# Kernel optimization log

Measured on AMD Instinct MI355X. Metric: run time of the kernel, lower is better.

## Reference

```python
import jax, jax.numpy as jnp
import numpy as np

MARGIN = 2.0
EPS = 1e-9


def setup_inputs() -> dict:
    key = jax.random.key(0)
    k1, k2 = jax.random.split(key)
    N, D, C = 8192, 128, 50
    outputs = jax.random.normal(k1, (N, D), dtype=jnp.float32)
    labels = jax.random.randint(k2, (N,), 0, C, dtype=jnp.int64)
    return {"outputs": outputs, "labels": labels}


def reference(outputs, labels):
    # Pairwise squared distances via Gram trick: ||xi||^2 + ||xj||^2 - 2 xi.xj
    sq = jnp.sum(outputs * outputs, axis=-1)  # [N]
    gram = outputs @ outputs.T                # [N, N]
    dist_sq = jnp.maximum(sq[:, None] + sq[None, :] - 2.0 * gram, 0.0)

    pos = (labels[:, None] == labels[None, :])  # includes i==j, as in original
    num_pos = jnp.sum(pos)
    num_neg = pos.size - num_pos

    dist_pos = jnp.sum(jnp.where(pos, dist_sq, 0.0))
    hinge = jax.nn.relu(MARGIN - jnp.sqrt(dist_sq + EPS))
    dist_neg = jnp.sum(jnp.where(pos, 0.0, hinge * hinge))

    pos_term = jnp.where(num_pos > 0, 0.5 * dist_pos / num_pos, 0.0)
    neg_term = jnp.where(num_neg > 0, 0.5 * dist_neg / num_neg, 0.0)
    return pos_term + neg_term
```

## Files before the change

kernel.cpp:

```cpp
#include <hip/hip_runtime.h>
#include <math.h>

#define NPTS   8192
#define DDIM   128
#define NBLK   64
#define NTRI   2080

using short8 = __attribute__((ext_vector_type(8))) short;
using f32x4  = __attribute__((ext_vector_type(4))) float;

__device__ __forceinline__ unsigned short f2bf(float f) {
    unsigned int u = __float_as_uint(f);
    u += 0x7fffu + ((u >> 16) & 1u);
    return (unsigned short)(u >> 16);
}
__device__ __forceinline__ float bf2f(unsigned short s) {
    return __uint_as_float(((unsigned int)s) << 16);
}

__global__ __launch_bounds__(256) void prep_kernel(
    const float* __restrict__ X, unsigned short* __restrict__ Xbf,
    float* __restrict__ sq)
{
    const int wave = threadIdx.x >> 6, lane = threadIdx.x & 63;
    const int row  = blockIdx.x * 4 + wave;
    float2 v = *(const float2*)(X + (size_t)row * DDIM + lane * 2);
    unsigned short a = f2bf(v.x), b = f2bf(v.y);
    float fa = bf2f(a), fb = bf2f(b);
    float s = fa * fa + fb * fb;
    *(ushort2*)(Xbf + (size_t)row * DDIM + lane * 2) = make_ushort2(a, b);
#pragma unroll
    for (int off = 32; off > 0; off >>= 1) s += __shfl_down(s, off);
    if (lane == 0) sq[row] = s;
}

__global__ __launch_bounds__(256) void pair_kernel(
    const unsigned short* __restrict__ Xbf, const int* __restrict__ lab,
    const float* __restrict__ sq, float* __restrict__ slots )
{
    const int k = blockIdx.x;
    int bi = (int)((129.0f - sqrtf((float)(16641 - 8 * k))) * 0.5f);
    if (bi < 0) bi = 0;
    while (64 * (bi + 1) - ((bi + 1) * bi) / 2 <= k) ++bi;
    while (64 * bi - (bi * (bi - 1)) / 2 > k) --bi;
    const int bj = bi + (k - (64 * bi - (bi * (bi - 1)) / 2));

    __shared__ float sSqA[128], sSqB[128];
    __shared__ int   sLabA[128], sLabB[128];
    __shared__ float rP[4], rN[4];

    const int tid   = threadIdx.x;
    const int rowA0 = bi * 128;
    const int rowB0 = bj * 128;

    if (tid < 128) {
        sSqA[tid]  = sq[rowA0 + tid];
        sLabA[tid] = lab[rowA0 + tid];
    } else {
        int t = tid - 128;
        sSqB[t]  = sq[rowB0 + t];
        sLabB[t] = lab[rowB0 + t];
    }
    __syncthreads();

    const int wave = tid >> 6, lane = tid & 63;
    const int quad = lane >> 4, rr = lane & 15;
    const int wr = wave >> 1, wc = wave & 1;

    const unsigned short* pA = Xbf + (size_t)(rowA0 + wr * 64 + rr) * DDIM + quad * 8;
    const unsigned short* pB = Xbf + (size_t)(rowB0 + wc * 64 + rr) * DDIM + quad * 8;

    f32x4 acc[4][4];
#pragma unroll
    for (int i = 0; i < 4; ++i)
#pragma unroll
        for (int j = 0; j < 4; ++j)
            acc[i][j] = (f32x4){0.f, 0.f, 0.f, 0.f};

#pragma unroll
    for (int kc = 0; kc < 4; ++kc) {
        short8 a[4], b[4];
#pragma unroll
        for (int t = 0; t < 4; ++t)
            a[t] = *(const short8*)(pA + t * 16 * DDIM + kc * 32);
#pragma unroll
        for (int t = 0; t < 4; ++t)
            b[t] = *(const short8*)(pB + t * 16 * DDIM + kc * 32);
#pragma unroll
        for (int i = 0; i < 4; ++i)
#pragma unroll
            for (int j = 0; j < 4; ++j)
                acc[i][j] = __builtin_amdgcn_mfma_f32_16x16x32_bf16(a[i], b[j], acc[i][j], 0, 0, 0);
    }

    float sb[4]; int lbv[4];
#pragma unroll
    for (int j = 0; j < 4; ++j) {
        int cl = wc * 64 + j * 16 + rr;
        sb[j] = sSqB[cl];
        lbv[j] = sLabB[cl];
    }

    float posS = 0.f, dmin = 1e30f;
#pragma unroll
    for (int i = 0; i < 4; ++i) {
#pragma unroll
        for (int rg = 0; rg < 4; ++rg) {
            int   rl = wr * 64 + i * 16 + quad * 4 + rg;
            float sa = sSqA[rl];
            int   la = sLabA[rl];
#pragma unroll
            for (int j = 0; j < 4; ++j) {
                float d = fmaxf(sa + sb[j] - 2.0f * acc[i][j][rg], 0.0f);
                bool same = (la == lbv[j]);
                posS += same ? d : 0.f;
                dmin = fminf(dmin, same ? 1e30f : d);
            }
        }
    }

    float negS = 0.f;
    if (__any(dmin + 1e-9f < 4.0f)) {
#pragma unroll
        for (int i = 0; i < 4; ++i) {
#pragma unroll
            for (int rg = 0; rg < 4; ++rg) {
                int   rl = wr * 64 + i * 16 + quad * 4 + rg;
                float sa = sSqA[rl];
                int   la = sLabA[rl];
#pragma unroll
                for (int j = 0; j < 4; ++j) {
                    float d = fmaxf(sa + sb[j] - 2.0f * acc[i][j][rg], 0.0f);
                    float t = fmaxf(2.0f - sqrtf(d + 1e-9f), 0.f);
                    negS += (la == lbv[j]) ? 0.f : t * t;
                }
            }
        }
    }

    const float factor = (bi == bj) ? 1.0f : 2.0f;
    posS *= factor; negS *= factor;

#pragma unroll
    for (int off = 32; off > 0; off >>= 1) {
        posS += __shfl_down(posS, off);
        negS += __shfl_down(negS, off);
    }
    if (lane == 0) { rP[wave] = posS; rN[wave] = negS; }
    __syncthreads();
    if (tid == 0) {
        slots[k]        = rP[0] + rP[1] + rP[2] + rP[3];
        slots[NTRI + k] = rN[0] + rN[1] + rN[2] + rN[3];
    }
}

__global__ __launch_bounds__(1024) void finalize_kernel(
    const float* __restrict__ slots, const int* __restrict__ lab,
    float* __restrict__ out)
{
    __shared__ int   hist[64];
    __shared__ float sP[16], sN[16];
    const int tid = threadIdx.x;
    if (tid < 64) hist[tid] = 0;
    __syncthreads();
    for (int i = tid; i < NPTS; i += 1024) atomicAdd(&hist[lab[i]], 1);

    float p = 0.f, n = 0.f;
    for (int i = tid; i < NTRI; i += 1024) { p += slots[i]; n += slots[NTRI + i]; }
#pragma unroll
    for (int off = 32; off > 0; off >>= 1) {
        p += __shfl_down(p, off);
        n += __shfl_down(n, off);
    }
    const int wave = tid >> 6, lane = tid & 63;
    if (lane == 0) { sP[wave] = p; sN[wave] = n; }
    __syncthreads();
    if (tid == 0) {
        long long np = 0;
        for (int c = 0; c < 64; ++c) np += (long long)hist[c] * hist[c];
        float tp = 0.f, tn = 0.f;
#pragma unroll
        for (int w = 0; w < 16; ++w) { tp += sP[w]; tn += sN[w]; }
        double dnp = (double)np;
        double dnn = (double)NPTS * (double)NPTS - dnp;
        double pt = (dnp > 0.0) ? 0.5 * (double)tp / dnp : 0.0;
        double nt = (dnn > 0.0) ? 0.5 * (double)tn / dnn : 0.0;
        out[0] = (float)(pt + nt);
    }
}

extern "C" void kernel_launch(void* const* d_in, const int* in_sizes, int n_in,
                              void* d_out, int out_size, void* d_ws, size_t ws_size,
                              hipStream_t stream) {
    const float* X   = (const float*)d_in[0];
    const int*   lab = (const int*)d_in[1];
    float*       out = (float*)d_out;

    char* ws = (char*)d_ws;
    unsigned short* Xbf   = (unsigned short*)(ws);
    float*          sq    = (float*)(ws + 2 * 1024 * 1024);
    float*          slots = (float*)(ws + 2 * 1024 * 1024 + 32 * 1024);

    prep_kernel<<<NPTS / 4, 256, 0, stream>>>(X, Xbf, sq);
    pair_kernel<<<NTRI, 256, 0, stream>>>(Xbf, lab, sq, slots);
    finalize_kernel<<<1, 1024, 0, stream>>>(slots, lab, out);
}
```

Before: 101.9 us.

## Compute positive-pair term from per-class sums and fuse finalize via last-block reduction

Replaces the per-pair positive-distance accumulation with a closed form built from per-class sums, squared norms and counts, which prep_kernel gathers with atomics. The pair kernel then computes only the minimum distance for its early-exit test and the negative hinge sum. A last-block-done counter folds the separate finalize kernel into the pair kernel. All A/B fragments are loaded up front before the MFMA loop, and launch bounds request two blocks per CU. In exchange it adds a memset, many global float atomics in prep, and a closed form in fp32 that can lose precision and differs slightly from using the bf16 Gram values.

```diff
diff --git a/kernel.cpp b/kernel.cpp
--- a/kernel.cpp
+++ b/kernel.cpp
@@ -19,24 +19,43 @@
 }
 
 __global__ __launch_bounds__(256) void prep_kernel(
-    const float* __restrict__ X, unsigned short* __restrict__ Xbf,
-    float* __restrict__ sq)
+    const float* __restrict__ X, const int* __restrict__ lab,
+    unsigned short* __restrict__ Xbf, float* __restrict__ sq,
+    float* __restrict__ clsSum, float* __restrict__ clsSq,
+    int* __restrict__ clsCnt)
 {
     const int wave = threadIdx.x >> 6, lane = threadIdx.x & 63;
     const int row  = blockIdx.x * 4 + wave;
+    const int c    = lab[row];
+
     float2 v = *(const float2*)(X + (size_t)row * DDIM + lane * 2);
     unsigned short a = f2bf(v.x), b = f2bf(v.y);
     float fa = bf2f(a), fb = bf2f(b);
-    float s = fa * fa + fb * fb;
+    float s_bf = fa * fa + fb * fb;
+    float s_fp = v.x * v.x + v.y * v.y;
     *(ushort2*)(Xbf + (size_t)row * DDIM + lane * 2) = make_ushort2(a, b);
-#pragma unroll
-    for (int off = 32; off > 0; off >>= 1) s += __shfl_down(s, off);
-    if (lane == 0) sq[row] = s;
-}
-
-__global__ __launch_bounds__(256) void pair_kernel(
+
+    atomicAdd(&clsSum[c * DDIM + lane * 2],     v.x);
+    atomicAdd(&clsSum[c * DDIM + lane * 2 + 1], v.y);
+
+#pragma unroll
+    for (int off = 32; off > 0; off >>= 1) {
+        s_bf += __shfl_down(s_bf, off);
+        s_fp += __shfl_down(s_fp, off);
+    }
+    if (lane == 0) {
+        sq[row] = s_bf;
+        atomicAdd(&clsSq[c], s_fp);
+        atomicAdd(clsCnt + c, 1);
+    }
+}
+
+__global__ __launch_bounds__(256, 2) void pair_kernel(
     const unsigned short* __restrict__ Xbf, const int* __restrict__ lab,
-    const float* __restrict__ sq, float* __restrict__ slots )
+    const float* __restrict__ sq, float* __restrict__ slots,
+    const float* __restrict__ clsSum, const float* __restrict__ clsSq,
+    const int* __restrict__ clsCnt, unsigned int* __restrict__ counter,
+    float* __restrict__ out)
 {
     const int k = blockIdx.x;
     int bi = (int)((129.0f - sqrtf((float)(16641 - 8 * k))) * 0.5f);
@@ -47,7 +66,8 @@
 
     __shared__ float sSqA[128], sSqB[128];
     __shared__ int   sLabA[128], sLabB[128];
-    __shared__ float rP[4], rN[4];
+    __shared__ float rN[4];
+    __shared__ int   sIsLast;
 
     const int tid   = threadIdx.x;
     const int rowA0 = bi * 128;
@@ -61,7 +81,6 @@
         sSqB[t]  = sq[rowB0 + t];
         sLabB[t] = lab[rowB0 + t];
     }
-    __syncthreads();
 
     const int wave = tid >> 6, lane = tid & 63;
     const int quad = lane >> 4, rr = lane & 15;
@@ -70,6 +89,16 @@
     const unsigned short* pA = Xbf + (size_t)(rowA0 + wr * 64 + rr) * DDIM + quad * 8;
     const unsigned short* pB = Xbf + (size_t)(rowB0 + wc * 64 + rr) * DDIM + quad * 8;
 
+    short8 a[4][4], b[4][4];
+#pragma unroll
+    for (int kc = 0; kc < 4; ++kc) {
+#pragma unroll
+        for (int t = 0; t < 4; ++t) {
+            a[t][kc] = *(const short8*)(pA + t * 16 * DDIM + kc * 32);
+            b[t][kc] = *(const short8*)(pB + t * 16 * DDIM + kc * 32);
+        }
+    }
+
     f32x4 acc[4][4];
 #pragma unroll
     for (int i = 0; i < 4; ++i)
@@ -78,49 +107,37 @@
             acc[i][j] = (f32x4){0.f, 0.f, 0.f, 0.f};
 
 #pragma unroll
-    for (int kc = 0; kc < 4; ++kc) {
-        short8 a[4], b[4];
-#pragma unroll
-        for (int t = 0; t < 4; ++t)
-            a[t] = *(const short8*)(pA + t * 16 * DDIM + kc * 32);
-#pragma unroll
-        for (int t = 0; t < 4; ++t)
-            b[t] = *(const short8*)(pB + t * 16 * DDIM + kc * 32);
+    for (int kc = 0; kc < 4; ++kc)
 #pragma unroll
         for (int i = 0; i < 4; ++i)
 #pragma unroll
             for (int j = 0; j < 4; ++j)
-                acc[i][j] = __builtin_amdgcn_mfma_f32_16x16x32_bf16(a[i], b[j], acc[i][j], 0, 0, 0);
-    }
-
-    float sb[4]; int lbv[4];
-#pragma unroll
-    for (int j = 0; j < 4; ++j) {
-        int cl = wc * 64 + j * 16 + rr;
-        sb[j] = sSqB[cl];
-        lbv[j] = sLabB[cl];
-    }
-
-    float posS = 0.f, dmin = 1e30f;
+                acc[i][j] = __builtin_amdgcn_mfma_f32_16x16x32_bf16(a[i][kc], b[j][kc], acc[i][j], 0, 0, 0);
+
+    __syncthreads();
+
+    float sb[4];
+#pragma unroll
+    for (int j = 0; j < 4; ++j) sb[j] = sSqB[wc * 64 + j * 16 + rr];
+
+    float dmin = 1e30f;
 #pragma unroll
     for (int i = 0; i < 4; ++i) {
-#pragma unroll
-        for (int rg = 0; rg < 4; ++rg) {
-            int   rl = wr * 64 + i * 16 + quad * 4 + rg;
-            float sa = sSqA[rl];
-            int   la = sLabA[rl];
-#pragma unroll
-            for (int j = 0; j < 4; ++j) {
-                float d = fmaxf(sa + sb[j] - 2.0f * acc[i][j][rg], 0.0f);
-                bool same = (la == lbv[j]);
-                posS += same ? d : 0.f;
-                dmin = fminf(dmin, same ? 1e30f : d);
-            }
-        }
+        float sa4[4];
+#pragma unroll
+        for (int rg = 0; rg < 4; ++rg) sa4[rg] = sSqA[wr * 64 + i * 16 + quad * 4 + rg];
+#pragma unroll
+        for (int rg = 0; rg < 4; ++rg)
+#pragma unroll
+            for (int j = 0; j < 4; ++j)
+                dmin = fminf(dmin, sa4[rg] + sb[j] - 2.0f * acc[i][j][rg]);
     }
 
     float negS = 0.f;
-    if (__any(dmin + 1e-9f < 4.0f)) {
+    if (__any(dmin < 4.0f)) {
+        int lb[4];
+#pragma unroll
+        for (int j = 0; j < 4; ++j) lb[j] = sLabB[wc * 64 + j * 16 + rr];
 #pragma unroll
         for (int i = 0; i < 4; ++i) {
 #pragma unroll
@@ -132,60 +149,59 @@
                 for (int j = 0; j < 4; ++j) {
                     float d = fmaxf(sa + sb[j] - 2.0f * acc[i][j][rg], 0.0f);
                     float t = fmaxf(2.0f - sqrtf(d + 1e-9f), 0.f);
-                    negS += (la == lbv[j]) ? 0.f : t * t;
+                    negS += (la == lb[j]) ? 0.f : t * t;
                 }
             }
         }
     }
 
-    const float factor = (bi == bj) ? 1.0f : 2.0f;
-    posS *= factor; negS *= factor;
-
+    negS *= (bi == bj) ? 1.0f : 2.0f;
+#pragma unroll
+    for (int off = 32; off > 0; off >>= 1) negS += __shfl_down(negS, off);
+    if (lane == 0) rN[wave] = negS;
+    __syncthreads();
+    if (tid == 0) {
+        slots[k] = rN[0] + rN[1] + rN[2] + rN[3];
+        __threadfence();
+        unsigned int old = atomicAdd(counter, 1);
+        sIsLast = (old == NTRI - 1);
+    }
+    __syncthreads();
+    if (!sIsLast) return;
+
+    __threadfence();
+    float nsum = 0.f;
+    for (int i = tid; i < NTRI; i += 256) nsum += slots[i];
+#pragma unroll
+    for (int off = 32; off > 0; off >>= 1) nsum += __shfl_down(nsum, off);
+    __syncthreads();
+    if (lane == 0) rN[wave] = nsum;
+    __syncthreads();
+
+    float pp = 0.f, np = 0.f;
+    if (tid < 64) {
+        float s2 = 0.f;
+        for (int d = 0; d < DDIM; ++d) {
+            float v = clsSum[tid * DDIM + d];
+            s2 = fmaf(v, v, s2);
+        }
+        float nc = (float)clsCnt[tid];
+        pp = nc * clsSq[tid] - s2;
+        np = nc * nc;
+    }
 #pragma unroll
     for (int off = 32; off > 0; off >>= 1) {
-        posS += __shfl_down(posS, off);
-        negS += __shfl_down(negS, off);
-    }
-    if (lane == 0) { rP[wave] = posS; rN[wave] = negS; }
-    __syncthreads();
+        pp += __shfl_down(pp, off);
+        np += __shfl_down(np, off);
+    }
     if (tid == 0) {
-        slots[k]        = rP[0] + rP[1] + rP[2] + rP[3];
-        slots[NTRI + k] = rN[0] + rN[1] + rN[2] + rN[3];
-    }
-}
-
-__global__ __launch_bounds__(1024) void finalize_kernel(
-    const float* __restrict__ slots, const int* __restrict__ lab,
-    float* __restrict__ out)
-{
-    __shared__ int   hist[64];
-    __shared__ float sP[16], sN[16];
-    const int tid = threadIdx.x;
-    if (tid < 64) hist[tid] = 0;
-    __syncthreads();
-    for (int i = tid; i < NPTS; i += 1024) atomicAdd(&hist[lab[i]], 1);
-
-    float p = 0.f, n = 0.f;
-    for (int i = tid; i < NTRI; i += 1024) { p += slots[i]; n += slots[NTRI + i]; }
-#pragma unroll
-    for (int off = 32; off > 0; off >>= 1) {
-        p += __shfl_down(p, off);
-        n += __shfl_down(n, off);
-    }
-    const int wave = tid >> 6, lane = tid & 63;
-    if (lane == 0) { sP[wave] = p; sN[wave] = n; }
-    __syncthreads();
-    if (tid == 0) {
-        long long np = 0;
-        for (int c = 0; c < 64; ++c) np += (long long)hist[c] * hist[c];
-        float tp = 0.f, tn = 0.f;
-#pragma unroll
-        for (int w = 0; w < 16; ++w) { tp += sP[w]; tn += sN[w]; }
-        double dnp = (double)np;
-        double dnn = (double)NPTS * (double)NPTS - dnp;
-        double pt = (dnp > 0.0) ? 0.5 * (double)tp / dnp : 0.0;
-        double nt = (dnn > 0.0) ? 0.5 * (double)tn / dnn : 0.0;
-        out[0] = (float)(pt + nt);
+        float  negTotal = rN[0] + rN[1] + rN[2] + rN[3];
+        double dist_pos = 2.0 * (double)pp;
+        double num_pos  = (double)np;
+        double num_neg  = (double)NPTS * (double)NPTS - num_pos;
+        double pos_t = (num_pos > 0.0) ? 0.5 * dist_pos / num_pos : 0.0;
+        double neg_t = (num_neg > 0.0) ? 0.5 * (double)negTotal / num_neg : 0.0;
+        out[0] = (float)(pos_t + neg_t);
     }
 }
 
@@ -197,11 +213,15 @@
     float*       out = (float*)d_out;
 
     char* ws = (char*)d_ws;
-    unsigned short* Xbf   = (unsigned short*)(ws);
-    float*          sq    = (float*)(ws + 2 * 1024 * 1024);
-    float*          slots = (float*)(ws + 2 * 1024 * 1024 + 32 * 1024);
-
-    prep_kernel<<<NPTS / 4, 256, 0, stream>>>(X, Xbf, sq);
-    pair_kernel<<<NTRI, 256, 0, stream>>>(Xbf, lab, sq, slots);
-    finalize_kernel<<<1, 1024, 0, stream>>>(slots, lab, out);
-}
+    unsigned int*   counter = (unsigned int*)(ws + 0);
+    int*            clsCnt  = (int*)(ws + 256);
+    float*          clsSq   = (float*)(ws + 1024);
+    float*          clsSum  = (float*)(ws + 4096);
+    float*          slots   = (float*)(ws + 64 * 1024);
+    float*          sq      = (float*)(ws + 80 * 1024);
+    unsigned short* Xbf     = (unsigned short*)(ws + 128 * 1024);
+
+    hipMemsetAsync(ws, 0, 64 * 1024, stream);
+    prep_kernel<<<NPTS / 4, 256, 0, stream>>>(X, lab, Xbf, sq, clsSum, clsSq, clsCnt);
+    pair_kernel<<<NTRI, 256, 0, stream>>>(Xbf, lab, sq, slots, clsSum, clsSq, clsCnt, counter, out);
+}
```

New measurement: 182.3 us. +78.9%, slower.

## Split pair tiles into per-wave 32x64 triangular tiles and drop LDS staging

Applied to the files above, without the earlier changes.

Each wave now handles its own 32x64 tile of the upper-triangular pair space, with 4 waves per block and 16512 wave tiles in total. Diagonal double counting is removed with an upper-strict mask, and the finalize step drops the 0.5 factor to match. This replaces the per-block shared-memory staging, __syncthreads and cross-wave reduction with direct global loads. The aim is to skip nearly half the redundant diagonal work, gain finer load balance and raise occupancy (launch_bounds 256,4). The cost is reloading B rows per wave instead of sharing them, and more slots for finalize to reduce.

```diff
diff --git a/kernel.cpp b/kernel.cpp
--- a/kernel.cpp
+++ b/kernel.cpp
@@ -3,8 +3,7 @@
 
 #define NPTS   8192
 #define DDIM   128
-#define NBLK   64
-#define NTRI   2080
+#define NT2    16512
 
 using short8 = __attribute__((ext_vector_type(8))) short;
 using f32x4  = __attribute__((ext_vector_type(4))) float;
@@ -16,6 +15,10 @@
 }
 __device__ __forceinline__ float bf2f(unsigned short s) {
     return __uint_as_float(((unsigned int)s) << 16);
+}
+
+__device__ __forceinline__ int Cof(int r) {
+    return 128 * r - ((r * r - 2 * r + (r & 1)) >> 2);
 }
 
 __global__ __launch_bounds__(256) void prep_kernel(
@@ -34,123 +37,113 @@
     if (lane == 0) sq[row] = s;
 }
 
-__global__ __launch_bounds__(256) void pair_kernel(
+__global__ __launch_bounds__(256, 4) void pair_kernel(
     const unsigned short* __restrict__ Xbf, const int* __restrict__ lab,
     const float* __restrict__ sq, float* __restrict__ slots )
 {
-    const int k = blockIdx.x;
-    int bi = (int)((129.0f - sqrtf((float)(16641 - 8 * k))) * 0.5f);
-    if (bi < 0) bi = 0;
-    while (64 * (bi + 1) - ((bi + 1) * bi) / 2 <= k) ++bi;
-    while (64 * bi - (bi * (bi - 1)) / 2 > k) --bi;
-    const int bj = bi + (k - (64 * bi - (bi * (bi - 1)) / 2));
-
-    __shared__ float sSqA[128], sSqB[128];
-    __shared__ int   sLabA[128], sLabB[128];
-    __shared__ float rP[4], rN[4];
-
-    const int tid   = threadIdx.x;
-    const int rowA0 = bi * 128;
-    const int rowB0 = bj * 128;
-
-    if (tid < 128) {
-        sSqA[tid]  = sq[rowA0 + tid];
-        sLabA[tid] = lab[rowA0 + tid];
-    } else {
-        int t = tid - 128;
-        sSqB[t]  = sq[rowB0 + t];
-        sLabB[t] = lab[rowB0 + t];
-    }
-    __syncthreads();
-
-    const int wave = tid >> 6, lane = tid & 63;
+    const int wave = threadIdx.x >> 6, lane = threadIdx.x & 63;
+    const int t = blockIdx.x * 4 + wave;
+
+    float s0 = sqrtf(264196.0f - 16.0f * (float)t);
+    int rb = (int)((514.0f - s0) * 0.5f);
+    if (rb < 0) rb = 0;
+    if (rb > 255) rb = 255;
+    while (Cof(rb + 1) <= t) ++rb;
+    while (Cof(rb) > t) --rb;
+    const int cb = (rb >> 1) + (t - Cof(rb));
+    const bool overlap = (cb == (rb >> 1));
+
     const int quad = lane >> 4, rr = lane & 15;
-    const int wr = wave >> 1, wc = wave & 1;
-
-    const unsigned short* pA = Xbf + (size_t)(rowA0 + wr * 64 + rr) * DDIM + quad * 8;
-    const unsigned short* pB = Xbf + (size_t)(rowB0 + wc * 64 + rr) * DDIM + quad * 8;
-
-    f32x4 acc[4][4];
-#pragma unroll
-    for (int i = 0; i < 4; ++i)
+    const int row0 = rb * 32, col0 = cb * 64;
+
+    const unsigned short* pA = Xbf + (size_t)(row0 + rr) * DDIM + quad * 8;
+    const unsigned short* pB = Xbf + (size_t)(col0 + rr) * DDIM + quad * 8;
+
+    f32x4 acc[2][4];
+#pragma unroll
+    for (int i = 0; i < 2; ++i)
 #pragma unroll
         for (int j = 0; j < 4; ++j)
             acc[i][j] = (f32x4){0.f, 0.f, 0.f, 0.f};
 
 #pragma unroll
     for (int kc = 0; kc < 4; ++kc) {
-        short8 a[4], b[4];
-#pragma unroll
-        for (int t = 0; t < 4; ++t)
-            a[t] = *(const short8*)(pA + t * 16 * DDIM + kc * 32);
-#pragma unroll
-        for (int t = 0; t < 4; ++t)
-            b[t] = *(const short8*)(pB + t * 16 * DDIM + kc * 32);
-#pragma unroll
-        for (int i = 0; i < 4; ++i)
+        short8 a[2], b[4];
+#pragma unroll
+        for (int i = 0; i < 2; ++i)
+            a[i] = *(const short8*)(pA + i * 16 * DDIM + kc * 32);
+#pragma unroll
+        for (int j = 0; j < 4; ++j)
+            b[j] = *(const short8*)(pB + j * 16 * DDIM + kc * 32);
+#pragma unroll
+        for (int i = 0; i < 2; ++i)
 #pragma unroll
             for (int j = 0; j < 4; ++j)
                 acc[i][j] = __builtin_amdgcn_mfma_f32_16x16x32_bf16(a[i], b[j], acc[i][j], 0, 0, 0);
     }
 
-    float sb[4]; int lbv[4];
+    float sb[4]; int lb[4];
 #pragma unroll
     for (int j = 0; j < 4; ++j) {
-        int cl = wc * 64 + j * 16 + rr;
-        sb[j] = sSqB[cl];
-        lbv[j] = sLabB[cl];
-    }
+        int cl = col0 + j * 16 + rr;
+        sb[j] = sq[cl];
+        lb[j] = lab[cl];
+    }
+    float sa[2][4]; int la[2][4];
+#pragma unroll
+    for (int i = 0; i < 2; ++i)
+#pragma unroll
+        for (int rg = 0; rg < 4; ++rg) {
+            int rl = row0 + i * 16 + quad * 4 + rg;
+            sa[i][rg] = sq[rl];
+            la[i][rg] = lab[rl];
+        }
 
     float posS = 0.f, dmin = 1e30f;
 #pragma unroll
-    for (int i = 0; i < 4; ++i) {
+    for (int i = 0; i < 2; ++i) {
 #pragma unroll
         for (int rg = 0; rg < 4; ++rg) {
-            int   rl = wr * 64 + i * 16 + quad * 4 + rg;
-            float sa = sSqA[rl];
-            int   la = sLabA[rl];
+            int rl = row0 + i * 16 + quad * 4 + rg;
 #pragma unroll
             for (int j = 0; j < 4; ++j) {
-                float d = fmaxf(sa + sb[j] - 2.0f * acc[i][j][rg], 0.0f);
-                bool same = (la == lbv[j]);
-                posS += same ? d : 0.f;
-                dmin = fminf(dmin, same ? 1e30f : d);
+                int   cl = col0 + j * 16 + rr;
+                bool  ok = !overlap || (cl > rl);
+                float d0 = sa[i][rg] + sb[j] - 2.0f * acc[i][j][rg];
+                bool  same = (la[i][rg] == lb[j]);
+                posS += (ok && same) ? fmaxf(d0, 0.f) : 0.f;
+                dmin = fminf(dmin, (ok && !same) ? d0 : 1e30f);
             }
         }
     }
 
     float negS = 0.f;
-    if (__any(dmin + 1e-9f < 4.0f)) {
-#pragma unroll
-        for (int i = 0; i < 4; ++i) {
+    if (__any(dmin < 4.0f)) {
+#pragma unroll
+        for (int i = 0; i < 2; ++i) {
 #pragma unroll
             for (int rg = 0; rg < 4; ++rg) {
-                int   rl = wr * 64 + i * 16 + quad * 4 + rg;
-                float sa = sSqA[rl];
-                int   la = sLabA[rl];
+                int rl = row0 + i * 16 + quad * 4 + rg;
 #pragma unroll
                 for (int j = 0; j < 4; ++j) {
-                    float d = fmaxf(sa + sb[j] - 2.0f * acc[i][j][rg], 0.0f);
-                    float t = fmaxf(2.0f - sqrtf(d + 1e-9f), 0.f);
-                    negS += (la == lbv[j]) ? 0.f : t * t;
+                    int   cl = col0 + j * 16 + rr;
+                    bool  ok = !overlap || (cl > rl);
+                    float d = fmaxf(sa[i][rg] + sb[j] - 2.0f * acc[i][j][rg], 0.f);
+                    float h = fmaxf(2.0f - sqrtf(d + 1e-9f), 0.f);
+                    negS += (ok && (la[i][rg] != lb[j])) ? h * h : 0.f;
                 }
             }
         }
     }
 
-    const float factor = (bi == bj) ? 1.0f : 2.0f;
-    posS *= factor; negS *= factor;
-
 #pragma unroll
     for (int off = 32; off > 0; off >>= 1) {
         posS += __shfl_down(posS, off);
         negS += __shfl_down(negS, off);
     }
-    if (lane == 0) { rP[wave] = posS; rN[wave] = negS; }
-    __syncthreads();
-    if (tid == 0) {
-        slots[k]        = rP[0] + rP[1] + rP[2] + rP[3];
-        slots[NTRI + k] = rN[0] + rN[1] + rN[2] + rN[3];
+    if (lane == 0) {
+        slots[t]       = posS;
+        slots[NT2 + t] = negS;
     }
 }
 
@@ -166,7 +159,7 @@
     for (int i = tid; i < NPTS; i += 1024) atomicAdd(&hist[lab[i]], 1);
 
     float p = 0.f, n = 0.f;
-    for (int i = tid; i < NTRI; i += 1024) { p += slots[i]; n += slots[NTRI + i]; }
+    for (int i = tid; i < NT2; i += 1024) { p += slots[i]; n += slots[NT2 + i]; }
 #pragma unroll
     for (int off = 32; off > 0; off >>= 1) {
         p += __shfl_down(p, off);
@@ -181,11 +174,11 @@
         float tp = 0.f, tn = 0.f;
 #pragma unroll
         for (int w = 0; w < 16; ++w) { tp += sP[w]; tn += sN[w]; }
-        double dnp = (double)np;
-        double dnn = (double)NPTS * (double)NPTS - dnp;
-        double pt = (dnp > 0.0) ? 0.5 * (double)tp / dnp : 0.0;
-        double nt = (dnn > 0.0) ? 0.5 * (double)tn / dnn : 0.0;
-        out[0] = (float)(pt + nt);
+        double num_pos = (double)np;
+        double num_neg = (double)NPTS * (double)NPTS - num_pos;
+        double pos_t = (num_pos > 0.0) ? (double)tp / num_pos : 0.0;
+        double neg_t = (num_neg > 0.0) ? (double)tn / num_neg : 0.0;
+        out[0] = (float)(pos_t + neg_t);
     }
 }
 
@@ -197,11 +190,11 @@
     float*       out = (float*)d_out;
 
     char* ws = (char*)d_ws;
-    unsigned short* Xbf   = (unsigned short*)(ws);
-    float*          sq    = (float*)(ws + 2 * 1024 * 1024);
-    float*          slots = (float*)(ws + 2 * 1024 * 1024 + 32 * 1024);
+    float*          slots = (float*)(ws);
+    float*          sq    = (float*)(ws + 160 * 1024);
+    unsigned short* Xbf   = (unsigned short*)(ws + 256 * 1024);
 
     prep_kernel<<<NPTS / 4, 256, 0, stream>>>(X, Xbf, sq);
-    pair_kernel<<<NTRI, 256, 0, stream>>>(Xbf, lab, sq, slots);
+    pair_kernel<<<NT2 / 4, 256, 0, stream>>>(Xbf, lab, sq, slots);
     finalize_kernel<<<1, 1024, 0, stream>>>(slots, lab, out);
 }
```

After: 117.4 us. 1.15x slower.

## Stage tiles via global_load_lds into swizzled LDS and fuse finalize via last-block counter

Applied to the files above, without the earlier changes.

Tiles of the bf16 matrix are copied directly from global into XOR-swizzled shared memory with async LDS loads, and the MFMA operands are then read from LDS instead of being loaded per wave from global memory. The separate finalize kernel is removed: each block atomically increments a counter and the last block does the histogram and final reduction, with the counter cleared by a memset. This is meant to cut duplicate global traffic and one kernel launch. In exchange it uses 64KB of LDS per block, which limits occupancy, and adds a serialized tail reduction in one block.

```diff
diff --git a/kernel.cpp b/kernel.cpp
--- a/kernel.cpp
+++ b/kernel.cpp
@@ -9,6 +9,9 @@
 using short8 = __attribute__((ext_vector_type(8))) short;
 using f32x4  = __attribute__((ext_vector_type(4))) float;
 
+typedef unsigned int as1_uint __attribute__((address_space(1)));
+typedef unsigned int as3_uint __attribute__((address_space(3)));
+
 __device__ __forceinline__ unsigned short f2bf(float f) {
     unsigned int u = __float_as_uint(f);
     u += 0x7fffu + ((u >> 16) & 1u);
@@ -16,6 +19,11 @@
 }
 __device__ __forceinline__ float bf2f(unsigned short s) {
     return __uint_as_float(((unsigned int)s) << 16);
+}
+
+__device__ __forceinline__ void gld16(const unsigned short* g, unsigned short* l) {
+    __builtin_amdgcn_global_load_lds(
+        (const as1_uint*)(const void*)g, (as3_uint*)(void*)l, 16, 0, 0);
 }
 
 __global__ __launch_bounds__(256) void prep_kernel(
@@ -34,9 +42,10 @@
     if (lane == 0) sq[row] = s;
 }
 
-__global__ __launch_bounds__(256) void pair_kernel(
+__global__ __launch_bounds__(256, 2) void pair_kernel(
     const unsigned short* __restrict__ Xbf, const int* __restrict__ lab,
-    const float* __restrict__ sq, float* __restrict__ slots )
+    const float* __restrict__ sq, float* __restrict__ slots,
+    unsigned int* __restrict__ counter, float* __restrict__ out)
 {
     const int k = blockIdx.x;
     int bi = (int)((129.0f - sqrtf((float)(16641 - 8 * k))) * 0.5f);
@@ -45,13 +54,33 @@
     while (64 * bi - (bi * (bi - 1)) / 2 > k) --bi;
     const int bj = bi + (k - (64 * bi - (bi * (bi - 1)) / 2));
 
+    __shared__ unsigned short sA[128 * 128];
+    __shared__ unsigned short sB[128 * 128];
     __shared__ float sSqA[128], sSqB[128];
     __shared__ int   sLabA[128], sLabB[128];
     __shared__ float rP[4], rN[4];
+    __shared__ int   sIsLast, sHist[64];
 
     const int tid   = threadIdx.x;
     const int rowA0 = bi * 128;
     const int rowB0 = bj * 128;
+
+    const unsigned short* gA = Xbf + (size_t)rowA0 * DDIM;
+    const unsigned short* gB = Xbf + (size_t)rowB0 * DDIM;
+#pragma unroll
+    for (int it = 0; it < 8; ++it) {
+        int g = it * 256 + tid;
+        int r = g >> 4, u = g & 15;
+        int c8 = u ^ (r & 7);
+        gld16(gA + r * DDIM + c8 * 8, sA + (size_t)g * 8);
+    }
+#pragma unroll
+    for (int it = 0; it < 8; ++it) {
+        int g = it * 256 + tid;
+        int r = g >> 4, u = g & 15;
+        int c8 = u ^ (r & 7);
+        gld16(gB + r * DDIM + c8 * 8, sB + (size_t)g * 8);
+    }
 
     if (tid < 128) {
         sSqA[tid]  = sq[rowA0 + tid];
@@ -67,9 +96,6 @@
     const int quad = lane >> 4, rr = lane & 15;
     const int wr = wave >> 1, wc = wave & 1;
 
-    const unsigned short* pA = Xbf + (size_t)(rowA0 + wr * 64 + rr) * DDIM + quad * 8;
-    const unsigned short* pB = Xbf + (size_t)(rowB0 + wc * 64 + rr) * DDIM + quad * 8;
-
     f32x4 acc[4][4];
 #pragma unroll
     for (int i = 0; i < 4; ++i)
@@ -80,12 +106,17 @@
 #pragma unroll
     for (int kc = 0; kc < 4; ++kc) {
         short8 a[4], b[4];
-#pragma unroll
-        for (int t = 0; t < 4; ++t)
-            a[t] = *(const short8*)(pA + t * 16 * DDIM + kc * 32);
-#pragma unroll
-        for (int t = 0; t < 4; ++t)
-            b[t] = *(const short8*)(pB + t * 16 * DDIM + kc * 32);
+        const int c8 = kc * 4 + quad;
+#pragma unroll
+        for (int t = 0; t < 4; ++t) {
+            int R = wr * 64 + t * 16 + rr;
+            a[t] = *(const short8*)&sA[R * 128 + ((c8 ^ (R & 7)) << 3)];
+        }
+#pragma unroll
+        for (int t = 0; t < 4; ++t) {
+            int R = wc * 64 + t * 16 + rr;
+            b[t] = *(const short8*)&sB[R * 128 + ((c8 ^ (R & 7)) << 3)];
+        }
 #pragma unroll
         for (int i = 0; i < 4; ++i)
 #pragma unroll
@@ -93,12 +124,12 @@
                 acc[i][j] = __builtin_amdgcn_mfma_f32_16x16x32_bf16(a[i], b[j], acc[i][j], 0, 0, 0);
     }
 
-    float sb[4]; int lbv[4];
+    float sb[4]; int lb[4];
 #pragma unroll
     for (int j = 0; j < 4; ++j) {
         int cl = wc * 64 + j * 16 + rr;
         sb[j] = sSqB[cl];
-        lbv[j] = sLabB[cl];
+        lb[j] = sLabB[cl];
     }
 
     float posS = 0.f, dmin = 1e30f;
@@ -111,16 +142,16 @@
             int   la = sLabA[rl];
 #pragma unroll
             for (int j = 0; j < 4; ++j) {
-                float d = fmaxf(sa + sb[j] - 2.0f * acc[i][j][rg], 0.0f);
-                bool same = (la == lbv[j]);
-                posS += same ? d : 0.f;
-                dmin = fminf(dmin, same ? 1e30f : d);
+                float d0 = sa + sb[j] - 2.0f * acc[i][j][rg];
+                bool  same = (la == lb[j]);
+                posS += same ? fmaxf(d0, 0.f) : 0.f;
+                dmin = fminf(dmin, same ? 1e30f : d0);
             }
         }
     }
 
     float negS = 0.f;
-    if (__any(dmin + 1e-9f < 4.0f)) {
+    if (__any(dmin < 4.0f)) {
 #pragma unroll
         for (int i = 0; i < 4; ++i) {
 #pragma unroll
@@ -130,9 +161,9 @@
                 int   la = sLabA[rl];
 #pragma unroll
                 for (int j = 0; j < 4; ++j) {
-                    float d = fmaxf(sa + sb[j] - 2.0f * acc[i][j][rg], 0.0f);
-                    float t = fmaxf(2.0f - sqrtf(d + 1e-9f), 0.f);
-                    negS += (la == lbv[j]) ? 0.f : t * t;
+                    float d = fmaxf(sa + sb[j] - 2.0f * acc[i][j][rg], 0.f);
+                    float h = fmaxf(2.0f - sqrtf(d + 1e-9f), 0.f);
+                    negS += (la == lb[j]) ? 0.f : h * h;
                 }
             }
         }
@@ -151,41 +182,37 @@
     if (tid == 0) {
         slots[k]        = rP[0] + rP[1] + rP[2] + rP[3];
         slots[NTRI + k] = rN[0] + rN[1] + rN[2] + rN[3];
-    }
-}
-
-__global__ __launch_bounds__(1024) void finalize_kernel(
-    const float* __restrict__ slots, const int* __restrict__ lab,
-    float* __restrict__ out)
-{
-    __shared__ int   hist[64];
-    __shared__ float sP[16], sN[16];
-    const int tid = threadIdx.x;
-    if (tid < 64) hist[tid] = 0;
-    __syncthreads();
-    for (int i = tid; i < NPTS; i += 1024) atomicAdd(&hist[lab[i]], 1);
+        __threadfence();
+        unsigned int old = atomicAdd(counter, 1);
+        sIsLast = (old == NTRI - 1);
+    }
+    __syncthreads();
+    if (!sIsLast) return;
+
+    __threadfence();
+    if (tid < 64) sHist[tid] = 0;
+    __syncthreads();
+    for (int i = tid; i < NPTS; i += 256) atomicAdd(&sHist[lab[i]], 1);
 
     float p = 0.f, n = 0.f;
-    for (int i = tid; i < NTRI; i += 1024) { p += slots[i]; n += slots[NTRI + i]; }
+    for (int i = tid; i < NTRI; i += 256) { p += slots[i]; n += slots[NTRI + i]; }
 #pragma unroll
     for (int off = 32; off > 0; off >>= 1) {
         p += __shfl_down(p, off);
         n += __shfl_down(n, off);
     }
-    const int wave = tid >> 6, lane = tid & 63;
-    if (lane == 0) { sP[wave] = p; sN[wave] = n; }
+    if (lane == 0) { rP[wave] = p; rN[wave] = n; }
     __syncthreads();
     if (tid == 0) {
         long long np = 0;
-        for (int c = 0; c < 64; ++c) np += (long long)hist[c] * hist[c];
-        float tp = 0.f, tn = 0.f;
-#pragma unroll
-        for (int w = 0; w < 16; ++w) { tp += sP[w]; tn += sN[w]; }
-        double dnp = (double)np;
-        double dnn = (double)NPTS * (double)NPTS - dnp;
-        double pt = (dnp > 0.0) ? 0.5 * (double)tp / dnp : 0.0;
-        double nt = (dnn > 0.0) ? 0.5 * (double)tn / dnn : 0.0;
-        out[0] = (float)(pt + nt);
+        for (int c = 0; c < 64; ++c) np += (long long)sHist[c] * sHist[c];
+        float tp = rP[0] + rP[1] + rP[2] + rP[3];
+        float tn = rN[0] + rN[1] + rN[2] + rN[3];
+        double num_pos = (double)np;
+        double num_neg = (double)NPTS * (double)NPTS - num_pos;
+        double pos_t = (num_pos > 0.0) ? 0.5 * (double)tp / num_pos : 0.0;
+        double neg_t = (num_neg > 0.0) ? 0.5 * (double)tn / num_neg : 0.0;
+        out[0] = (float)(pos_t + neg_t);
     }
 }
 
@@ -197,11 +224,12 @@
     float*       out = (float*)d_out;
 
     char* ws = (char*)d_ws;
-    unsigned short* Xbf   = (unsigned short*)(ws);
-    float*          sq    = (float*)(ws + 2 * 1024 * 1024);
-    float*          slots = (float*)(ws + 2 * 1024 * 1024 + 32 * 1024);
-
+    unsigned int*   counter = (unsigned int*)(ws + 0);
+    float*          slots   = (float*)(ws + 256);
+    float*          sq      = (float*)(ws + 20 * 1024);
+    unsigned short* Xbf     = (unsigned short*)(ws + 64 * 1024);
+
+    hipMemsetAsync(ws, 0, 256, stream);
     prep_kernel<<<NPTS / 4, 256, 0, stream>>>(X, Xbf, sq);
-    pair_kernel<<<NTRI, 256, 0, stream>>>(Xbf, lab, sq, slots);
-    finalize_kernel<<<1, 1024, 0, stream>>>(slots, lab, out);
-}
+    pair_kernel<<<NTRI, 256, 0, stream>>>(Xbf, lab, sq, slots, counter, out);
+}
```

New measurement: 123.9 us. 1.22x slower.
